# Kernel optimization log

Measured on AMD Instinct MI355X. Metric: run time of the kernel, lower is better.

Reference implementation:

```python
import jax, jax.numpy as jnp
import numpy as np

B, R, N, E, D, H = 4, 10, 64, 64, 300, 512  # batch, rounds, nodes, neighbours(=nodes), numberbatch_dim, lstm_hidden
SLOPE = 0.2  # LeakyReLU negative slope from config['slope']


def _xavier_uniform(key, shape, gain=1.414):
    fan_in, fan_out = shape[0], shape[1]
    lim = gain * np.sqrt(6.0 / (fan_in + fan_out))
    return jax.random.uniform(key, shape, jnp.float32, -lim, lim)


def setup_inputs() -> dict:
    key = jax.random.key(0)
    k0, k1, k2, k3, k4 = jax.random.split(key, 5)
    return {
        "adj_list": jax.random.normal(k0, (B, R, N, E, D), jnp.float32),
        "original_nodes": jax.random.normal(k1, (B, R, N, D), jnp.float32),
        "ques_embed": jax.random.normal(k2, (B, R, H), jnp.float32),
        "W": _xavier_uniform(k3, (D + H, H)),
        "a": _xavier_uniform(k4, (2 * H, 1)),
    }


def reference(adj_list, original_nodes, ques_embed, W, a):
    d_in = original_nodes.shape[-1]
    h = W.shape[-1]
    # Split W so that concat([x, q]) @ W == x @ Wn + q @ Wq (avoids the explicit
    # repeat + concat in the original torch code; same math).
    Wn, Wq = W[:d_in], W[d_in:]
    q_proj = jnp.einsum('brq,qh->brh', ques_embed, Wq)              # (B,R,H)
    w_original = jnp.einsum('brnd,dh->brnh', original_nodes, Wn) + q_proj[:, :, None, :]      # (B,R,N,H)
    Wh = jnp.einsum('brned,dh->brneh', adj_list, Wn) + q_proj[:, :, None, None, :]            # (B,R,N,E,H)
    a1, a2 = a[:h, 0], a[h:, 0]
    # e[b,r,n,e] = leakyrelu( (w_original @ a1)[b,r,n] + (Wh @ a2)[b,r,n,e] )
    scores = jnp.einsum('brnh,h->brn', w_original, a1)[..., None] + jnp.einsum('brneh,h->brne', Wh, a2)
    scores = jnp.where(scores > 0, scores, SLOPE * scores)
    # Faithful to original: softmax over dim=1 (the rounds axis). Dropout omitted (eval mode).
    attn = jax.nn.softmax(scores, axis=1)                            # (B,R,N,E)
    # h_prime[b,r,i,h] = sum_j attn[b,r,i,j] * w_original[b,r,j,h]  (requires E == N)
    h_prime = jnp.einsum('brij,brjh->brih', attn, w_original)
    return jax.nn.elu(h_prime)  # concat=True branch
```

## Files before the change

kernel.cpp:

```cpp
#include <hip/hip_runtime.h>
#include <math.h>

namespace {
constexpr int B = 4, R = 10, N = 64, E = 64, D = 300, H = 512;
constexpr int BR = B * R;
constexpr int NE = N * E;
constexpr int S = BR * NE;
constexpr float SLOPE = 0.2f;
constexpr int ATTN_BLOCKS = 1024;
constexpr int ATTN_WAVES = ATTN_BLOCKS * 4;
constexpr int UPW = (B * NE) / ATTN_WAVES;

constexpr int OFF_V1  = 0;
constexpr int OFF_V2  = OFF_V1 + 300;
constexpr int OFF_U1  = OFF_V2 + 300;
constexpr int OFF_U2  = OFF_U1 + H;
constexpr int OFF_QP  = OFF_U2 + H;
constexpr int OFF_QA1 = OFF_QP + BR * H;
constexpr int OFF_QA2 = OFF_QA1 + BR;
constexpr int OFF_S1  = OFF_QA2 + BR;
constexpr int OFF_SC  = OFF_S1 + BR * N;
constexpr int OFF_WO  = OFF_SC + S;
}

__device__ inline float waveReduce(float v) {
#pragma unroll
  for (int o = 32; o > 0; o >>= 1) v += __shfl_xor(v, o, 64);
  return v;
}

__device__ inline float dot4(float4 a, float4 b) {
  return a.x * b.x + a.y * b.y + a.z * b.z + a.w * b.w;
}

__global__ __launch_bounds__(64) void k_vecs(const float* __restrict__ W,
                                             const float* __restrict__ a,
                                             float* __restrict__ ws) {
  int row = blockIdx.x;
  int lane = threadIdx.x;
  const float4* rf  = reinterpret_cast<const float4*>(W + (size_t)row * H);
  const float4* a1f = reinterpret_cast<const float4*>(a);
  const float4* a2f = reinterpret_cast<const float4*>(a + H);
  float4 x0 = rf[lane], x1 = rf[64 + lane];
  float4 p0 = a1f[lane], p1 = a1f[64 + lane];
  float4 q0 = a2f[lane], q1 = a2f[64 + lane];
  float s1 = dot4(x0, p0) + dot4(x1, p1);
  float s2 = dot4(x0, q0) + dot4(x1, q1);
  s1 = waveReduce(s1);
  s2 = waveReduce(s2);
  if (lane == 0) {
    if (row < D) { ws[OFF_V1 + row] = s1; ws[OFF_V2 + row] = s2; }
    else         { ws[OFF_U1 + (row - D)] = s1; ws[OFF_U2 + (row - D)] = s2; }
  }
}

__global__ __launch_bounds__(512) void k_qproj_s1(const float* __restrict__ ques,
                                                  const float* __restrict__ W,
                                                  const float* __restrict__ orig,
                                                  float* __restrict__ ws) {
  int br = blockIdx.x, h = threadIdx.x;
  __shared__ float qs[H];
  __shared__ float red[16];
  __shared__ float qa1s;
  qs[h] = ques[(size_t)br * H + h];
  __syncthreads();
  float ac0 = 0.f, ac1 = 0.f, ac2 = 0.f, ac3 = 0.f;
#pragma unroll 4
  for (int q = 0; q < H; q += 4) {
    ac0 = fmaf(qs[q + 0], W[(size_t)(D + q + 0) * H + h], ac0);
    ac1 = fmaf(qs[q + 1], W[(size_t)(D + q + 1) * H + h], ac1);
    ac2 = fmaf(qs[q + 2], W[(size_t)(D + q + 2) * H + h], ac2);
    ac3 = fmaf(qs[q + 3], W[(size_t)(D + q + 3) * H + h], ac3);
  }
  float acc = (ac0 + ac1) + (ac2 + ac3);
  ws[OFF_QP + br * H + h] = acc;
  float p1 = qs[h] * ws[OFF_U1 + h];
  float p2 = qs[h] * ws[OFF_U2 + h];
  p1 = waveReduce(p1);
  p2 = waveReduce(p2);
  int lane = h & 63, wave = h >> 6;
  if (lane == 0) { red[wave] = p1; red[8 + wave] = p2; }
  __syncthreads();
  if (h == 0) {
    float t1 = 0.f, t2 = 0.f;
#pragma unroll
    for (int i = 0; i < 8; ++i) { t1 += red[i]; t2 += red[8 + i]; }
    ws[OFF_QA1 + br] = t1;
    ws[OFF_QA2 + br] = t2;
    qa1s = t1;
  }
  __syncthreads();
  float qa1 = qa1s;
  const float4* vf = reinterpret_cast<const float4*>(ws + OFF_V1);
  float4 va = vf[lane];
  float4 vb = (lane < 11) ? vf[64 + lane] : make_float4(0.f, 0.f, 0.f, 0.f);
  for (int n2 = wave * 8; n2 < wave * 8 + 8; n2 += 2) {
    const float4* rf0 = reinterpret_cast<const float4*>(orig + ((size_t)br * N + n2) * D);
    const float4* rf1 = reinterpret_cast<const float4*>(orig + ((size_t)br * N + n2 + 1) * D);
    float a0 = dot4(rf0[lane], va);
    float a1 = dot4(rf1[lane], va);
    if (lane < 11) {
      a0 += dot4(rf0[64 + lane], vb);
      a1 += dot4(rf1[64 + lane], vb);
    }
#pragma unroll
    for (int o = 32; o > 0; o >>= 1) {
      a0 += __shfl_xor(a0, o, 64);
      a1 += __shfl_xor(a1, o, 64);
    }
    if (lane == 0) {
      ws[OFF_S1 + br * N + n2]     = a0 + qa1;
      ws[OFF_S1 + br * N + n2 + 1] = a1 + qa1;
    }
  }
}

__global__ __launch_bounds__(512) void k_wo(const float* __restrict__ orig,
                                            const float* __restrict__ W,
                                            float* __restrict__ ws) {
  int br = blockIdx.x >> 3, h0 = (blockIdx.x & 7) * 64;
  int t = threadIdx.x;
  __shared__ __align__(16) float sA[64 * 60];
  __shared__ __align__(16) float sB[60 * 64];
  const float4* sBf = reinterpret_cast<const float4*>(sB);
  int tn = t >> 4, th = t & 15;
  float acc[2][4] = {};
  for (int k0 = 0; k0 < D; k0 += 60) {
    __syncthreads();
    for (int idx = t; idx < 64 * 60; idx += 512) {
      int n = idx / 60, kk = idx % 60;
      sA[idx] = orig[((size_t)br * N + n) * D + k0 + kk];
    }
    for (int idx = t; idx < 60 * 64; idx += 512) {
      int kk = idx >> 6, hh = idx & 63;
      sB[idx] = W[(size_t)(k0 + kk) * H + h0 + hh];
    }
    __syncthreads();
#pragma unroll 4
    for (int kk = 0; kk < 60; ++kk) {
      float av0 = sA[(tn * 2 + 0) * 60 + kk];
      float av1 = sA[(tn * 2 + 1) * 60 + kk];
      float4 bv = sBf[kk * 16 + th];
      acc[0][0] = fmaf(av0, bv.x, acc[0][0]);
      acc[0][1] = fmaf(av0, bv.y, acc[0][1]);
      acc[0][2] = fmaf(av0, bv.z, acc[0][2]);
      acc[0][3] = fmaf(av0, bv.w, acc[0][3]);
      acc[1][0] = fmaf(av1, bv.x, acc[1][0]);
      acc[1][1] = fmaf(av1, bv.y, acc[1][1]);
      acc[1][2] = fmaf(av1, bv.z, acc[1][2]);
      acc[1][3] = fmaf(av1, bv.w, acc[1][3]);
    }
  }
#pragma unroll
  for (int i = 0; i < 2; ++i) {
    int n = tn * 2 + i;
#pragma unroll
    for (int j = 0; j < 4; ++j) {
      int h = h0 + th * 4 + j;
      ws[OFF_WO + ((size_t)br * N + n) * H + h] = acc[i][j] + ws[OFF_QP + br * H + h];
    }
  }
}

__device__ __forceinline__ void attn_load_x(const float* __restrict__ adj, int u,
                                            int lane, float4 (&x)[R]) {
  const float* base = adj + ((size_t)(u >> 12) * R * NE + (u & 4095)) * D;
#pragma unroll
  for (int r = 0; r < R; ++r)
    x[r] = reinterpret_cast<const float4*>(base + (size_t)r * NE * D)[lane];
}

__device__ __forceinline__ void attn_compute(const float* __restrict__ adj,
                                             float* __restrict__ ws, int u, int lane,
                                             const float4 (&x)[R],
                                             float4 va, float4 vb) {
  int b = u >> 12, ne = u & 4095, n = ne >> 6, brb = b * R;
  const float* base = adj + ((size_t)b * R * NE + ne) * D;
  bool tl = lane < 11;
  float4 y[R];
  if (tl) {
#pragma unroll
    for (int r = 0; r < R; ++r)
      y[r] = reinterpret_cast<const float4*>(base + (size_t)r * NE * D)[64 + lane];
  }
  float add[R];
#pragma unroll
  for (int r = 0; r < R; ++r)
    add[r] = ws[OFF_QA2 + brb + r] + ws[OFF_S1 + (brb + r) * N + n];
  float acc[R];
#pragma unroll
  for (int r = 0; r < R; ++r) acc[r] = dot4(x[r], va);
  if (tl) {
#pragma unroll
    for (int r = 0; r < R; ++r) acc[r] += dot4(y[r], vb);
  }
#pragma unroll
  for (int o = 32; o > 0; o >>= 1) {
#pragma unroll
    for (int r = 0; r < R; ++r) acc[r] += __shfl_xor(acc[r], o, 64);
  }
  float m = -1e30f;
#pragma unroll
  for (int r = 0; r < R; ++r) {
    float sc = acc[r] + add[r];
    sc = sc > 0.f ? sc : SLOPE * sc;
    acc[r] = sc;
    m = fmaxf(m, sc);
  }
  float s = 0.f;
#pragma unroll
  for (int r = 0; r < R; ++r) { acc[r] = __expf(acc[r] - m); s += acc[r]; }
  float inv = 1.f / s;
  if (lane == 0) {
#pragma unroll
    for (int r = 0; r < R; ++r)
      ws[OFF_SC + (size_t)(brb + r) * NE + ne] = acc[r] * inv;
  }
}

__global__ __launch_bounds__(256) void k_attn(const float* __restrict__ adj,
                                              float* __restrict__ ws) {
  int aw = blockIdx.x * 4 + (threadIdx.x >> 6);
  int lane = threadIdx.x & 63;
  const float4* vf = reinterpret_cast<const float4*>(ws + OFF_V2);
  float4 va = vf[lane];
  float4 vb = (lane < 11) ? vf[64 + lane] : make_float4(0.f, 0.f, 0.f, 0.f);
  float4 xA[R], xB[R];
  attn_load_x(adj, aw, lane, xA);
#pragma unroll
  for (int i = 0; i < UPW; ++i) {
    int u = aw + i * ATTN_WAVES;
    if (i + 1 < UPW) {
      if (i & 1) attn_load_x(adj, aw + (i + 1) * ATTN_WAVES, lane, xA);
      else       attn_load_x(adj, aw + (i + 1) * ATTN_WAVES, lane, xB);
    }
    if (i & 1) attn_compute(adj, ws, u, lane, xB, va, vb);
    else       attn_compute(adj, ws, u, lane, xA, va, vb);
  }
}

__global__ __launch_bounds__(256) void k_hprime(const float* __restrict__ ws,
                                                float* __restrict__ out) {
  int br = blockIdx.x;
  int h = blockIdx.y * 64 + (threadIdx.x & 63);
  int ig = threadIdx.x >> 6;
  __shared__ __align__(16) float sAtt[64 * 64];
  const float* att = ws + OFF_SC + (size_t)br * NE;
  for (int idx = threadIdx.x; idx < 4096; idx += 256) sAtt[idx] = att[idx];
  __syncthreads();
  float acc[16] = {};
  const float* wo = ws + OFF_WO + (size_t)br * N * H;
  const float4* sAttf = reinterpret_cast<const float4*>(sAtt);
#pragma unroll 2
  for (int j4 = 0; j4 < 16; ++j4) {
    float w0 = wo[(size_t)(4 * j4 + 0) * H + h];
    float w1 = wo[(size_t)(4 * j4 + 1) * H + h];
    float w2 = wo[(size_t)(4 * j4 + 2) * H + h];
    float w3 = wo[(size_t)(4 * j4 + 3) * H + h];
#pragma unroll
    for (int ii = 0; ii < 16; ++ii) {
      float4 a4 = sAttf[(ig * 16 + ii) * 16 + j4];
      acc[ii] = fmaf(a4.x, w0, fmaf(a4.y, w1, fmaf(a4.z, w2, fmaf(a4.w, w3, acc[ii]))));
    }
  }
#pragma unroll
  for (int ii = 0; ii < 16; ++ii) {
    int i = ig * 16 + ii;
    float x = acc[ii];
    out[((size_t)br * N + i) * H + h] = x > 0.f ? x : expm1f(x);
  }
}

extern "C" void kernel_launch(void* const* d_in, const int* in_sizes, int n_in,
                              void* d_out, int out_size, void* d_ws, size_t ws_size,
                              hipStream_t stream) {
  const float* adj  = (const float*)d_in[0];
  const float* orig = (const float*)d_in[1];
  const float* ques = (const float*)d_in[2];
  const float* W    = (const float*)d_in[3];
  const float* a    = (const float*)d_in[4];
  float* out = (float*)d_out;
  float* ws  = (float*)d_ws;

  k_vecs<<<dim3(D + H), dim3(64), 0, stream>>>(W, a, ws);
  k_qproj_s1<<<dim3(BR), dim3(512), 0, stream>>>(ques, W, orig, ws);
  k_wo<<<dim3(BR * 8), dim3(512), 0, stream>>>(orig, W, ws);
  k_attn<<<dim3(ATTN_BLOCKS), dim3(256), 0, stream>>>(adj, ws);
  k_hprime<<<dim3(BR, 8), dim3(256), 0, stream>>>(ws, out);
}
```

Baseline: 114.2 us.

## Split attention into contiguous-slab dot kernel and separate rounds softmax

```diff
diff --git a/kernel.cpp b/kernel.cpp
--- a/kernel.cpp
+++ b/kernel.cpp
@@ -7,9 +7,8 @@
 constexpr int NE = N * E;
 constexpr int S = BR * NE;
 constexpr float SLOPE = 0.2f;
-constexpr int ATTN_BLOCKS = 1024;
-constexpr int ATTN_WAVES = ATTN_BLOCKS * 4;
-constexpr int UPW = (B * NE) / ATTN_WAVES;
+constexpr int S2_ROWS = 32;
+constexpr int S2_BLOCKS = S / S2_ROWS;
 
 constexpr int OFF_V1  = 0;
 constexpr int OFF_V2  = OFF_V1 + 300;
@@ -19,7 +18,8 @@
 constexpr int OFF_QA1 = OFF_QP + BR * H;
 constexpr int OFF_QA2 = OFF_QA1 + BR;
 constexpr int OFF_S1  = OFF_QA2 + BR;
-constexpr int OFF_SC  = OFF_S1 + BR * N;
+constexpr int OFF_RAW = OFF_S1 + BR * N;
+constexpr int OFF_SC  = OFF_RAW + S;
 constexpr int OFF_WO  = OFF_SC + S;
 }
 
@@ -162,81 +162,56 @@
   }
 }
 
-__device__ __forceinline__ void attn_load_x(const float* __restrict__ adj, int u,
-                                            int lane, float4 (&x)[R]) {
-  const float* base = adj + ((size_t)(u >> 12) * R * NE + (u & 4095)) * D;
+__global__ __launch_bounds__(256) void k_s2(const float* __restrict__ adj,
+                                            float* __restrict__ ws) {
+  __shared__ __align__(16) float4 slab[S2_ROWS * 77];
+  int t = threadIdx.x;
+  const float4* src = reinterpret_cast<const float4*>(adj) + (size_t)blockIdx.x * (S2_ROWS * 75);
+  for (int i = t; i < S2_ROWS * 75; i += 256) {
+    slab[(i / 75) * 77 + (i % 75)] = src[i];
+  }
+  __syncthreads();
+  int row = t >> 3, g = t & 7;
+  const float4* v4 = reinterpret_cast<const float4*>(ws + OFF_V2);
+  float acc = 0.f;
+#pragma unroll
+  for (int k = 0; k < 10; ++k) {
+    int j = g + 8 * k;
+    if (j < 75) {
+      float4 x = slab[row * 77 + j];
+      float4 v = v4[j];
+      acc = fmaf(x.x, v.x, fmaf(x.y, v.y, fmaf(x.z, v.z, fmaf(x.w, v.w, acc))));
+    }
+  }
+  acc += __shfl_xor(acc, 1, 64);
+  acc += __shfl_xor(acc, 2, 64);
+  acc += __shfl_xor(acc, 4, 64);
+  if (g == 0) ws[OFF_RAW + (size_t)blockIdx.x * S2_ROWS + row] = acc;
+}
+
+__global__ __launch_bounds__(256) void k_softmax(float* __restrict__ ws) {
+  int t = blockIdx.x * 256 + threadIdx.x;
+  int b = t >> 12;
+  int ne = t & 4095;
+  int n = ne >> 6;
+  const float* raw = ws + OFF_RAW;
+  float v[R];
+  float m = -1e30f;
+#pragma unroll
+  for (int r = 0; r < R; ++r) {
+    int br = b * R + r;
+    float sc = raw[(size_t)br * NE + ne] + ws[OFF_QA2 + br] + ws[OFF_S1 + br * N + n];
+    sc = sc > 0.f ? sc : SLOPE * sc;
+    v[r] = sc;
+    m = fmaxf(m, sc);
+  }
+  float s = 0.f;
+#pragma unroll
+  for (int r = 0; r < R; ++r) { v[r] = __expf(v[r] - m); s += v[r]; }
+  float inv = 1.f / s;
 #pragma unroll
   for (int r = 0; r < R; ++r)
-    x[r] = reinterpret_cast<const float4*>(base + (size_t)r * NE * D)[lane];
-}
-
-__device__ __forceinline__ void attn_compute(const float* __restrict__ adj,
-                                             float* __restrict__ ws, int u, int lane,
-                                             const float4 (&x)[R],
-                                             float4 va, float4 vb) {
-  int b = u >> 12, ne = u & 4095, n = ne >> 6, brb = b * R;
-  const float* base = adj + ((size_t)b * R * NE + ne) * D;
-  bool tl = lane < 11;
-  float4 y[R];
-  if (tl) {
-#pragma unroll
-    for (int r = 0; r < R; ++r)
-      y[r] = reinterpret_cast<const float4*>(base + (size_t)r * NE * D)[64 + lane];
-  }
-  float add[R];
-#pragma unroll
-  for (int r = 0; r < R; ++r)
-    add[r] = ws[OFF_QA2 + brb + r] + ws[OFF_S1 + (brb + r) * N + n];
-  float acc[R];
-#pragma unroll
-  for (int r = 0; r < R; ++r) acc[r] = dot4(x[r], va);
-  if (tl) {
-#pragma unroll
-    for (int r = 0; r < R; ++r) acc[r] += dot4(y[r], vb);
-  }
-#pragma unroll
-  for (int o = 32; o > 0; o >>= 1) {
-#pragma unroll
-    for (int r = 0; r < R; ++r) acc[r] += __shfl_xor(acc[r], o, 64);
-  }
-  float m = -1e30f;
-#pragma unroll
-  for (int r = 0; r < R; ++r) {
-    float sc = acc[r] + add[r];
-    sc = sc > 0.f ? sc : SLOPE * sc;
-    acc[r] = sc;
-    m = fmaxf(m, sc);
-  }
-  float s = 0.f;
-#pragma unroll
-  for (int r = 0; r < R; ++r) { acc[r] = __expf(acc[r] - m); s += acc[r]; }
-  float inv = 1.f / s;
-  if (lane == 0) {
-#pragma unroll
-    for (int r = 0; r < R; ++r)
-      ws[OFF_SC + (size_t)(brb + r) * NE + ne] = acc[r] * inv;
-  }
-}
-
-__global__ __launch_bounds__(256) void k_attn(const float* __restrict__ adj,
-                                              float* __restrict__ ws) {
-  int aw = blockIdx.x * 4 + (threadIdx.x >> 6);
-  int lane = threadIdx.x & 63;
-  const float4* vf = reinterpret_cast<const float4*>(ws + OFF_V2);
-  float4 va = vf[lane];
-  float4 vb = (lane < 11) ? vf[64 + lane] : make_float4(0.f, 0.f, 0.f, 0.f);
-  float4 xA[R], xB[R];
-  attn_load_x(adj, aw, lane, xA);
-#pragma unroll
-  for (int i = 0; i < UPW; ++i) {
-    int u = aw + i * ATTN_WAVES;
-    if (i + 1 < UPW) {
-      if (i & 1) attn_load_x(adj, aw + (i + 1) * ATTN_WAVES, lane, xA);
-      else       attn_load_x(adj, aw + (i + 1) * ATTN_WAVES, lane, xB);
-    }
-    if (i & 1) attn_compute(adj, ws, u, lane, xB, va, vb);
-    else       attn_compute(adj, ws, u, lane, xA, va, vb);
-  }
+    ws[OFF_SC + (size_t)(b * R + r) * NE + ne] = v[r] * inv;
 }
 
 __global__ __launch_bounds__(256) void k_hprime(const float* __restrict__ ws,
@@ -285,6 +260,7 @@
   k_vecs<<<dim3(D + H), dim3(64), 0, stream>>>(W, a, ws);
   k_qproj_s1<<<dim3(BR), dim3(512), 0, stream>>>(ques, W, orig, ws);
   k_wo<<<dim3(BR * 8), dim3(512), 0, stream>>>(orig, W, ws);
-  k_attn<<<dim3(ATTN_BLOCKS), dim3(256), 0, stream>>>(adj, ws);
+  k_s2<<<dim3(S2_BLOCKS), dim3(256), 0, stream>>>(adj, ws);
+  k_softmax<<<dim3(B * NE / 256), dim3(256), 0, stream>>>(ws);
   k_hprime<<<dim3(BR, 8), dim3(256), 0, stream>>>(ws, out);
 }
```

After: 112.6 us. Within noise of the previous version (-1.4%).
